# Kernel optimization log

Hardware: AMD Instinct MI355X
Metric: run time of the kernel (lower is better)

The kernel has to match this reference:

```python
import jax, jax.numpy as jnp
import numpy as np
from jax import lax

B, S, C, H, P = 128, 512, 64, 512, 192  # batch, seq_len, enc_in, hidden_size, pred_len


def setup_inputs() -> dict:
    key = jax.random.key(0)
    ks = jax.random.split(key, 9)
    s_enc = 1.0 / np.sqrt(C)
    s_lstm = 1.0 / np.sqrt(H)
    return {
        "x": jax.random.normal(ks[0], (B, S, C), dtype=jnp.float32),
        "enc_W": jax.random.uniform(ks[1], (H, C), jnp.float32, -s_enc, s_enc),
        "enc_b": jax.random.uniform(ks[2], (H,), jnp.float32, -s_enc, s_enc),
        "Wih": jax.random.uniform(ks[3], (4 * H, H), jnp.float32, -s_lstm, s_lstm),
        "Whh": jax.random.uniform(ks[4], (4 * H, H), jnp.float32, -s_lstm, s_lstm),
        "bih": jax.random.uniform(ks[5], (4 * H,), jnp.float32, -s_lstm, s_lstm),
        "bhh": jax.random.uniform(ks[6], (4 * H,), jnp.float32, -s_lstm, s_lstm),
        "dec_W": jax.random.uniform(ks[7], (C, H), jnp.float32, -s_lstm, s_lstm),
        "dec_b": jax.random.uniform(ks[8], (C,), jnp.float32, -s_lstm, s_lstm),
    }


def _gates(pre):
    # PyTorch LSTM gate order: i, f, g, o
    i, f, g, o = jnp.split(pre, 4, axis=-1)
    return jax.nn.sigmoid(i), jax.nn.sigmoid(f), jnp.tanh(g), jax.nn.sigmoid(o)


def reference(x, enc_W, enc_b, Wih, Whh, bih, bhh, dec_W, dec_b):
    b = bih + bhh

    # encoder: [B,S,C] -> [B,S,H]
    xe = x @ enc_W.T + enc_b

    # main LSTM over seq_len with zero init state
    def cell(carry, xt):
        h, c = carry
        i, f, g, o = _gates(xt @ Wih.T + h @ Whh.T + b)
        c2 = f * c + i * g
        h2 = o * jnp.tanh(c2)
        return (h2, c2), h2

    z = jnp.zeros((x.shape[0], Wih.shape[0] // 4), dtype=x.dtype)
    (_, _), outs = lax.scan(cell, (z, z), xe.transpose(1, 0, 2))  # outs: [S,B,H]
    h_last = outs[-1]

    # (torch code calls self.Lstm(h) without passing (h,c)), fed previous h.
    def step(h_prev, _):
        i, f, g, o = _gates(h_prev @ Wih.T + b)  # h-state=0 -> no Whh term
        c2 = i * g  # f*0 + i*g
        h2 = o * jnp.tanh(c2)
        return h2, h2

    _, preds = lax.scan(step, h_last, None, length=P)  # [P,B,H]

    full = jnp.concatenate([outs, preds], axis=0)[1:]  # drop first step: [S+P-1,B,H]
    out = full.transpose(1, 0, 2) @ dec_W.T + dec_b  # [B, S+P-1, C]
    return out
```

## Files before the change

kernel.cpp:

```cpp
#include <hip/hip_runtime.h>
#include <cstdint>
#include <cstddef>


typedef __bf16 bf16x8 __attribute__((ext_vector_type(8)));
typedef float  f32x4  __attribute__((ext_vector_type(4)));

static constexpr unsigned long long SENT = 0x7FC07FC07FC07FC0ULL;

static constexpr size_t SZ_HALL = (size_t)705 * 128 * 512 * 2;
static constexpr size_t SZ_WCAT = (size_t)2048 * 576 * 2;
static constexpr size_t SZ_WIH  = (size_t)2048 * 512 * 2;
static constexpr size_t SZ_DECW = (size_t)64 * 512 * 2;
static constexpr size_t SZ_XT   = (size_t)512 * 128 * 64 * 2;
static constexpr size_t OFF_HALL = 0;
static constexpr size_t OFF_WCAT = OFF_HALL + SZ_HALL;
static constexpr size_t OFF_WIH  = OFF_WCAT + SZ_WCAT;
static constexpr size_t OFF_DECW = OFF_WIH + SZ_WIH;
static constexpr size_t OFF_XT   = OFF_DECW + SZ_DECW;
static constexpr size_t OFF_B2   = OFF_XT + SZ_XT;
static constexpr size_t OFF_BAR_ = OFF_B2 + 2048 * 4;
static constexpr size_t WS_NEEDED = OFF_BAR_ + 2048 * 4;

__device__ __forceinline__ float sigm(float x) { return 1.f / (1.f + __expf(-x)); }
__device__ __forceinline__ float tanh_fast(float x) {
  return 1.f - 2.f / (__expf(2.f * x) + 1.f);
}

__global__ void __launch_bounds__(256)
setup0(const float* __restrict__ x, const float* __restrict__ Wih,
       const float* __restrict__ Whh, const float* __restrict__ bih,
       const float* __restrict__ bhh, const float* __restrict__ decW,
       __bf16* __restrict__ xT, __bf16* __restrict__ Wih_bf,
       __bf16* __restrict__ Wcat, __bf16* __restrict__ decW_bf,
       float* __restrict__ b_ar, __bf16* __restrict__ h_all)
{
  size_t gid = (size_t)blockIdx.x * blockDim.x + threadIdx.x;
  size_t gsz = (size_t)gridDim.x * blockDim.x;
  for (size_t i = gid; i < 4194304u; i += gsz) {
    size_t t = i >> 13, b = (i >> 6) & 127u, c = i & 63u;
    xT[i] = (__bf16)x[(b * 512 + t) * 64 + c];
  }
  for (size_t i = gid; i < 1048576u; i += gsz) Wih_bf[i] = (__bf16)Wih[i];
  for (size_t i = gid; i < 1048576u; i += gsz) {
    size_t r = i >> 9, k = i & 511u;
    Wcat[r * 576 + k] = (__bf16)Whh[i];
  }
  for (size_t i = gid; i < 32768u; i += gsz) decW_bf[i] = (__bf16)decW[i];
  for (size_t i = gid; i < 2048u; i += gsz) b_ar[i] = bih[i] + bhh[i];
  unsigned long long* hp = (unsigned long long*)h_all;
  for (size_t i = gid; i < 16384u; i += gsz) hp[i] = 0ULL;
  for (size_t i = 16384u + gid; i < 11550720u; i += gsz) hp[i] = SENT;
}

__global__ void __launch_bounds__(64)
setup1(const float* __restrict__ Wih, const float* __restrict__ encW,
       const float* __restrict__ encb, const float* __restrict__ bih,
       const float* __restrict__ bhh, __bf16* __restrict__ Wcat,
       float* __restrict__ b2)
{
  int r = blockIdx.x;
  int c = threadIdx.x;
  const float* wr = Wih + (size_t)r * 512;
  float acc = 0.f;
  for (int k = 0; k < 512; ++k) acc += wr[k] * encW[(size_t)k * 64 + c];
  Wcat[(size_t)r * 576 + 512 + c] = (__bf16)acc;
  float p = 0.f;
  for (int kk = 0; kk < 8; ++kk) { int k = kk * 64 + c; p += wr[k] * encb[k]; }
  for (int off = 32; off > 0; off >>= 1) p += __shfl_down(p, off);
  if (c == 0) b2[r] = bih[r] + bhh[r] + p;
}

template<bool MAIN>
__device__ __forceinline__ void lstm_step(
    unsigned t, int tid, int wv, int lane, int n16, int quad, int b0, int f0,
    const bf16x8 (&wf)[18], const f32x4& bv,
    __bf16* __restrict__ h_all, const __bf16* __restrict__ xT,
    float& creg, __bf16 (&A)[16][584], __bf16 (&hb)[16][68])
{
  uint4 xv;
  if (MAIN && tid < 128)
    xv = *(const uint4*)(xT + (size_t)(t - 1) * 8192 +
                         (size_t)(b0 + (tid >> 3)) * 64 + (tid & 7) * 8);

  const unsigned long long* src = (const unsigned long long*)
      (h_all + (size_t)(t - 1) * 65536 + (size_t)(b0 + (tid >> 6)) * 512) +
      (size_t)(tid & 63) * 2;
  unsigned long long v0 = __hip_atomic_load(src,     __ATOMIC_RELAXED, __HIP_MEMORY_SCOPE_AGENT);
  unsigned long long v1 = __hip_atomic_load(src + 1, __ATOMIC_RELAXED, __HIP_MEMORY_SCOPE_AGENT);
  while (v0 == SENT || v1 == SENT) {
    if (v0 == SENT) v0 = __hip_atomic_load(src,     __ATOMIC_RELAXED, __HIP_MEMORY_SCOPE_AGENT);
    if (v1 == SENT) v1 = __hip_atomic_load(src + 1, __ATOMIC_RELAXED, __HIP_MEMORY_SCOPE_AGENT);
  }

  {
    unsigned long long* ad = (unsigned long long*)&A[tid >> 6][(tid & 63) * 8];
    ad[0] = v0; ad[1] = v1;
  }
  if (MAIN && tid < 128)
    *(uint4*)(&A[tid >> 3][512 + (tid & 7) * 8]) = xv;
  __syncthreads();

  f32x4 a0 = bv, a1 = {0.f, 0.f, 0.f, 0.f};
  const __bf16* arow = &A[n16][quad * 8];
  #pragma unroll
  for (int kc = 0; kc < (MAIN ? 18 : 16); ++kc) {
    bf16x8 af = *(const bf16x8*)(arow + kc * 32);
    if (kc & 1) a1 = __builtin_amdgcn_mfma_f32_16x16x32_bf16(wf[kc], af, a1, 0, 0, 0);
    else        a0 = __builtin_amdgcn_mfma_f32_16x16x32_bf16(wf[kc], af, a0, 0, 0, 0);
  }
  a0 += a1;

  float ig = sigm(a0[0]), gg = tanh_fast(a0[2]), og = sigm(a0[3]);
  float c2;
  if (MAIN) { float fg = sigm(a0[1]); c2 = fg * creg + ig * gg; creg = c2; }
  else      { c2 = ig * gg; }
  hb[n16][wv * 4 + quad] = (__bf16)(og * tanh_fast(c2));
  __syncthreads();

  if (tid < 256) {
    const int em = tid >> 4, p = tid & 15;
    unsigned long long pk = *(const unsigned long long*)&hb[em][p * 4];
    unsigned long long* dst = (unsigned long long*)
        (h_all + (size_t)t * 65536 + (size_t)(b0 + em) * 512 + f0) + p;
    __hip_atomic_store(dst, pk, __ATOMIC_RELAXED, __HIP_MEMORY_SCOPE_AGENT);
  }
}

__global__ void __launch_bounds__(1024, 4)
lstm_persist(const __bf16* __restrict__ xT, const __bf16* __restrict__ Wcat,
             const __bf16* __restrict__ Wih_bf, const float* __restrict__ b2,
             const float* __restrict__ b_ar, __bf16* __restrict__ h_all)
{
  const int bid = blockIdx.x;
  const int g = bid & 7, sub = bid >> 3;
  const int b0 = g * 16, f0 = sub * 64;
  const int tid = threadIdx.x;
  const int wv = tid >> 6, lane = tid & 63;
  const int n16 = lane & 15, quad = lane >> 4;

  __shared__ __align__(16) __bf16 A[16][584];
  __shared__ __align__(16) __bf16 hb[16][68];

  bf16x8 wf[18];
  f32x4 bv;
  {
    const int gate = n16 & 3, fl = n16 >> 2;
    const __bf16* wrow = Wcat + (size_t)(gate * 512 + f0 + wv * 4 + fl) * 576 + quad * 8;
    #pragma unroll
    for (int kc = 0; kc < 18; ++kc) wf[kc] = *(const bf16x8*)(wrow + kc * 32);
    const int fb = f0 + wv * 4 + quad;
    bv = f32x4{b2[fb], b2[512 + fb], b2[1024 + fb], b2[1536 + fb]};
  }

  float creg = 0.f;

  for (unsigned t = 1; t <= 512; ++t)
    lstm_step<true>(t, tid, wv, lane, n16, quad, b0, f0, wf, bv,
                    h_all, xT, creg, A, hb);

  {
    const int gate = n16 & 3, fl = n16 >> 2;
    const __bf16* wrow = Wih_bf + (size_t)(gate * 512 + f0 + wv * 4 + fl) * 512 + quad * 8;
    #pragma unroll
    for (int kc = 0; kc < 16; ++kc) wf[kc] = *(const bf16x8*)(wrow + kc * 32);
    const int fb = f0 + wv * 4 + quad;
    bv = f32x4{b_ar[fb], b_ar[512 + fb], b_ar[1024 + fb], b_ar[1536 + fb]};
  }
  for (unsigned t = 513; t <= 704; ++t)
    lstm_step<false>(t, tid, wv, lane, n16, quad, b0, f0, wf, bv,
                     h_all, xT, creg, A, hb);
}

__global__ void __launch_bounds__(256)
final_proj(const __bf16* __restrict__ h_all, const __bf16* __restrict__ decW_bf,
           const float* __restrict__ decb, float* __restrict__ out)
{
  const int bi = blockIdx.x;
  const int tid = threadIdx.x;
  const int wv = tid >> 6, lane = tid & 63;
  const int n16 = lane & 15, quad = lane >> 4;
  const size_t r0 = 256 + (size_t)bi * 128 + (size_t)wv * 32;

  f32x4 acc[2][4];
  #pragma unroll
  for (int mt = 0; mt < 2; ++mt)
    #pragma unroll
    for (int nt = 0; nt < 4; ++nt) acc[mt][nt] = f32x4{0.f, 0.f, 0.f, 0.f};

  const __bf16* arow0 = h_all + (r0 + n16) * 512 + quad * 8;
  const __bf16* arow1 = arow0 + 16 * 512;
  const __bf16* brow  = decW_bf + (size_t)n16 * 512 + quad * 8;

  #pragma unroll
  for (int kc = 0; kc < 16; ++kc) {
    bf16x8 a0 = *(const bf16x8*)(arow0 + kc * 32);
    bf16x8 a1 = *(const bf16x8*)(arow1 + kc * 32);
    #pragma unroll
    for (int nt = 0; nt < 4; ++nt) {
      bf16x8 b = *(const bf16x8*)(brow + (size_t)nt * 8192 + kc * 32);
      acc[0][nt] = __builtin_amdgcn_mfma_f32_16x16x32_bf16(a0, b, acc[0][nt], 0, 0, 0);
      acc[1][nt] = __builtin_amdgcn_mfma_f32_16x16x32_bf16(a1, b, acc[1][nt], 0, 0, 0);
    }
  }
  #pragma unroll
  for (int mt = 0; mt < 2; ++mt)
    #pragma unroll
    for (int nt = 0; nt < 4; ++nt)
      #pragma unroll
      for (int r = 0; r < 4; ++r) {
        size_t R = r0 + mt * 16 + quad * 4 + r;
        int slot = (int)(R >> 7), b = (int)(R & 127);
        int j = slot - 2;
        int c = nt * 16 + n16;
        out[((size_t)b * 703 + j) * 64 + c] = acc[mt][nt][r] + decb[c];
      }
}

extern "C" void kernel_launch(void* const* d_in, const int* in_sizes, int n_in,
                              void* d_out, int out_size, void* d_ws, size_t ws_size,
                              hipStream_t stream)
{
  const float* x    = (const float*)d_in[0];
  const float* encW = (const float*)d_in[1];
  const float* encb = (const float*)d_in[2];
  const float* Wih  = (const float*)d_in[3];
  const float* Whh  = (const float*)d_in[4];
  const float* bih  = (const float*)d_in[5];
  const float* bhh  = (const float*)d_in[6];
  const float* decW = (const float*)d_in[7];
  const float* decb = (const float*)d_in[8];
  float* out = (float*)d_out;

  if (ws_size < WS_NEEDED) return;

  char* ws = (char*)d_ws;
  __bf16* h_all   = (__bf16*)(ws + OFF_HALL);
  __bf16* Wcat    = (__bf16*)(ws + OFF_WCAT);
  __bf16* Wih_bf  = (__bf16*)(ws + OFF_WIH);
  __bf16* decW_bf = (__bf16*)(ws + OFF_DECW);
  __bf16* xT      = (__bf16*)(ws + OFF_XT);
  float*  b2      = (float*)(ws + OFF_B2);
  float*  b_ar    = (float*)(ws + OFF_BAR_);

  hipLaunchKernelGGL(setup0, dim3(2048), dim3(256), 0, stream,
                     x, Wih, Whh, bih, bhh, decW, xT, Wih_bf, Wcat, decW_bf,
                     b_ar, h_all);
  hipLaunchKernelGGL(setup1, dim3(2048), dim3(64), 0, stream,
                     Wih, encW, encb, bih, bhh, Wcat, b2);
  hipLaunchKernelGGL(lstm_persist, dim3(64), dim3(1024), 0, stream,
                     xT, Wcat, Wih_bf, b2, b_ar, h_all);
  hipLaunchKernelGGL(final_proj, dim3(703), dim3(256), 0, stream,
                     h_all, decW_bf, decb, out);
}
```

Measured before the change: 1.840 ms.

## Split LSTM step K-reduction across wave pairs with LDS partial-sum exchange

Each wave now computes half of the K dimension for its own gate tile and half for its partner wave (wv^8), then the pair exchanges partial accumulators through a new shared buffer. Every wave still issues the same number of MFMAs, but the two independent accumulators per wave now cover different output tiles, and each wave reads only half of the A row from LDS. The goal is to shorten the dependent MFMA chain and the LDS read traffic on the serial per-step critical path. The cost is an extra __syncthreads and an LDS round trip of partial sums every timestep.

```diff
diff --git a/kernel.cpp b/kernel.cpp
--- a/kernel.cpp
+++ b/kernel.cpp
@@ -74,10 +74,15 @@
 template<bool MAIN>
 __device__ __forceinline__ void lstm_step(
     unsigned t, int tid, int wv, int lane, int n16, int quad, int b0, int f0,
-    const bf16x8 (&wf)[18], const f32x4& bv,
+    const bf16x8 (&wfo)[9], const bf16x8 (&wfx)[9], const f32x4& bv,
     __bf16* __restrict__ h_all, const __bf16* __restrict__ xT,
-    float& creg, __bf16 (&A)[16][584], __bf16 (&hb)[16][68])
-{
+    float& creg, __bf16 (&A)[16][584], __bf16 (&hb)[16][68],
+    f32x4 (&px)[8][2][64])
+{
+  const int p = wv & 7, r = wv >> 3;
+  const int kb = r * (MAIN ? 9 : 8);
+  constexpr int KH = MAIN ? 9 : 8;
+
   uint4 xv;
   if (MAIN && tid < 128)
     xv = *(const uint4*)(xT + (size_t)(t - 1) * 8192 +
@@ -101,28 +106,31 @@
     *(uint4*)(&A[tid >> 3][512 + (tid & 7) * 8]) = xv;
   __syncthreads();
 
-  f32x4 a0 = bv, a1 = {0.f, 0.f, 0.f, 0.f};
-  const __bf16* arow = &A[n16][quad * 8];
-  #pragma unroll
-  for (int kc = 0; kc < (MAIN ? 18 : 16); ++kc) {
+  f32x4 ao = bv, ax = {0.f, 0.f, 0.f, 0.f};
+  const __bf16* arow = &A[n16][quad * 8 + kb * 32];
+  #pragma unroll
+  for (int kc = 0; kc < KH; ++kc) {
     bf16x8 af = *(const bf16x8*)(arow + kc * 32);
-    if (kc & 1) a1 = __builtin_amdgcn_mfma_f32_16x16x32_bf16(wf[kc], af, a1, 0, 0, 0);
-    else        a0 = __builtin_amdgcn_mfma_f32_16x16x32_bf16(wf[kc], af, a0, 0, 0, 0);
-  }
-  a0 += a1;
-
-  float ig = sigm(a0[0]), gg = tanh_fast(a0[2]), og = sigm(a0[3]);
+    ao = __builtin_amdgcn_mfma_f32_16x16x32_bf16(wfo[kc], af, ao, 0, 0, 0);
+    ax = __builtin_amdgcn_mfma_f32_16x16x32_bf16(wfx[kc], af, ax, 0, 0, 0);
+  }
+
+  px[p][r][lane] = ax;
+  __syncthreads();
+  ao += px[p][r ^ 1][lane];
+
+  float ig = sigm(ao[0]), gg = tanh_fast(ao[2]), og = sigm(ao[3]);
   float c2;
-  if (MAIN) { float fg = sigm(a0[1]); c2 = fg * creg + ig * gg; creg = c2; }
+  if (MAIN) { float fg = sigm(ao[1]); c2 = fg * creg + ig * gg; creg = c2; }
   else      { c2 = ig * gg; }
   hb[n16][wv * 4 + quad] = (__bf16)(og * tanh_fast(c2));
   __syncthreads();
 
   if (tid < 256) {
-    const int em = tid >> 4, p = tid & 15;
-    unsigned long long pk = *(const unsigned long long*)&hb[em][p * 4];
+    const int em = tid >> 4, pp = tid & 15;
+    unsigned long long pk = *(const unsigned long long*)&hb[em][pp * 4];
     unsigned long long* dst = (unsigned long long*)
-        (h_all + (size_t)t * 65536 + (size_t)(b0 + em) * 512 + f0) + p;
+        (h_all + (size_t)t * 65536 + (size_t)(b0 + em) * 512 + f0) + pp;
     __hip_atomic_store(dst, pk, __ATOMIC_RELAXED, __HIP_MEMORY_SCOPE_AGENT);
   }
 }
@@ -141,14 +149,22 @@
 
   __shared__ __align__(16) __bf16 A[16][584];
   __shared__ __align__(16) __bf16 hb[16][68];
-
-  bf16x8 wf[18];
+  __shared__ __align__(16) f32x4 px[8][2][64];
+
+  bf16x8 wfo[9], wfx[9];
   f32x4 bv;
   {
     const int gate = n16 & 3, fl = n16 >> 2;
-    const __bf16* wrow = Wcat + (size_t)(gate * 512 + f0 + wv * 4 + fl) * 576 + quad * 8;
-    #pragma unroll
-    for (int kc = 0; kc < 18; ++kc) wf[kc] = *(const bf16x8*)(wrow + kc * 32);
+    const int kb = (wv >> 3) * 9;
+    const __bf16* wro = Wcat + (size_t)(gate * 512 + f0 + wv * 4 + fl) * 576
+                        + kb * 32 + quad * 8;
+    const __bf16* wrx = Wcat + (size_t)(gate * 512 + f0 + (wv ^ 8) * 4 + fl) * 576
+                        + kb * 32 + quad * 8;
+    #pragma unroll
+    for (int kc = 0; kc < 9; ++kc) {
+      wfo[kc] = *(const bf16x8*)(wro + kc * 32);
+      wfx[kc] = *(const bf16x8*)(wrx + kc * 32);
+    }
     const int fb = f0 + wv * 4 + quad;
     bv = f32x4{b2[fb], b2[512 + fb], b2[1024 + fb], b2[1536 + fb]};
   }
@@ -156,20 +172,27 @@
   float creg = 0.f;
 
   for (unsigned t = 1; t <= 512; ++t)
-    lstm_step<true>(t, tid, wv, lane, n16, quad, b0, f0, wf, bv,
-                    h_all, xT, creg, A, hb);
+    lstm_step<true>(t, tid, wv, lane, n16, quad, b0, f0, wfo, wfx, bv,
+                    h_all, xT, creg, A, hb, px);
 
   {
     const int gate = n16 & 3, fl = n16 >> 2;
-    const __bf16* wrow = Wih_bf + (size_t)(gate * 512 + f0 + wv * 4 + fl) * 512 + quad * 8;
-    #pragma unroll
-    for (int kc = 0; kc < 16; ++kc) wf[kc] = *(const bf16x8*)(wrow + kc * 32);
+    const int kb = (wv >> 3) * 8;
+    const __bf16* wro = Wih_bf + (size_t)(gate * 512 + f0 + wv * 4 + fl) * 512
+                        + kb * 32 + quad * 8;
+    const __bf16* wrx = Wih_bf + (size_t)(gate * 512 + f0 + (wv ^ 8) * 4 + fl) * 512
+                        + kb * 32 + quad * 8;
+    #pragma unroll
+    for (int kc = 0; kc < 8; ++kc) {
+      wfo[kc] = *(const bf16x8*)(wro + kc * 32);
+      wfx[kc] = *(const bf16x8*)(wrx + kc * 32);
+    }
     const int fb = f0 + wv * 4 + quad;
     bv = f32x4{b_ar[fb], b_ar[512 + fb], b_ar[1024 + fb], b_ar[1536 + fb]};
   }
   for (unsigned t = 513; t <= 704; ++t)
-    lstm_step<false>(t, tid, wv, lane, n16, quad, b0, f0, wf, bv,
-                     h_all, xT, creg, A, hb);
+    lstm_step<false>(t, tid, wv, lane, n16, quad, b0, f0, wfo, wfx, bv,
+                     h_all, xT, creg, A, hb, px);
 }
 
 __global__ void __launch_bounds__(256)
```

New measurement: 1.798 ms. 1.02x faster.

## Split LSTM over 128 smaller blocks with feature-quad-major h layout and shuffles

Applied to the files above, without the earlier changes.

The persistent LSTM kernel now runs 128 blocks of 512 threads, each owning 32 hidden features instead of 64, spreading the recurrence over more CUs. The h state buffer is relaid out as [t][feature-quad][batch] 8-byte words, so each wave packs its four gate-lane outputs with cross-lane shuffles and publishes them directly, removing the hb staging buffer and one __syncthreads per step. The A staging tile is double-buffered across steps, and final_proj is rewritten to read the new layout. The trade-off is more blocks polling flags each step and more strided 8-byte loads in the projection.

```diff
diff --git a/kernel.cpp b/kernel.cpp
--- a/kernel.cpp
+++ b/kernel.cpp
@@ -27,6 +27,7 @@
   return 1.f - 2.f / (__expf(2.f * x) + 1.f);
 }
 
+
 __global__ void __launch_bounds__(256)
 setup0(const float* __restrict__ x, const float* __restrict__ Wih,
        const float* __restrict__ Whh, const float* __restrict__ bih,
@@ -76,26 +77,30 @@
     unsigned t, int tid, int wv, int lane, int n16, int quad, int b0, int f0,
     const bf16x8 (&wf)[18], const f32x4& bv,
     __bf16* __restrict__ h_all, const __bf16* __restrict__ xT,
-    float& creg, __bf16 (&A)[16][584], __bf16 (&hb)[16][68])
+    float& creg, __bf16 (*A)[584])
 {
   uint4 xv;
   if (MAIN && tid < 128)
     xv = *(const uint4*)(xT + (size_t)(t - 1) * 8192 +
                          (size_t)(b0 + (tid >> 3)) * 64 + (tid & 7) * 8);
 
-  const unsigned long long* src = (const unsigned long long*)
-      (h_all + (size_t)(t - 1) * 65536 + (size_t)(b0 + (tid >> 6)) * 512) +
-      (size_t)(tid & 63) * 2;
-  unsigned long long v0 = __hip_atomic_load(src,     __ATOMIC_RELAXED, __HIP_MEMORY_SCOPE_AGENT);
-  unsigned long long v1 = __hip_atomic_load(src + 1, __ATOMIC_RELAXED, __HIP_MEMORY_SCOPE_AGENT);
-  while (v0 == SENT || v1 == SENT) {
-    if (v0 == SENT) v0 = __hip_atomic_load(src,     __ATOMIC_RELAXED, __HIP_MEMORY_SCOPE_AGENT);
-    if (v1 == SENT) v1 = __hip_atomic_load(src + 1, __ATOMIC_RELAXED, __HIP_MEMORY_SCOPE_AGENT);
+  const unsigned long long* s0 = (const unsigned long long*)
+      (h_all + (size_t)(t - 1) * 65536) +
+      (size_t)(wv * 16 + (quad << 2)) * 128 + (b0 + n16);
+  unsigned long long v0 = __hip_atomic_load(s0,       __ATOMIC_RELAXED, __HIP_MEMORY_SCOPE_AGENT);
+  unsigned long long v1 = __hip_atomic_load(s0 + 128, __ATOMIC_RELAXED, __HIP_MEMORY_SCOPE_AGENT);
+  unsigned long long v2 = __hip_atomic_load(s0 + 256, __ATOMIC_RELAXED, __HIP_MEMORY_SCOPE_AGENT);
+  unsigned long long v3 = __hip_atomic_load(s0 + 384, __ATOMIC_RELAXED, __HIP_MEMORY_SCOPE_AGENT);
+  while (v0 == SENT || v1 == SENT || v2 == SENT || v3 == SENT) {
+    if (v0 == SENT) v0 = __hip_atomic_load(s0,       __ATOMIC_RELAXED, __HIP_MEMORY_SCOPE_AGENT);
+    if (v1 == SENT) v1 = __hip_atomic_load(s0 + 128, __ATOMIC_RELAXED, __HIP_MEMORY_SCOPE_AGENT);
+    if (v2 == SENT) v2 = __hip_atomic_load(s0 + 256, __ATOMIC_RELAXED, __HIP_MEMORY_SCOPE_AGENT);
+    if (v3 == SENT) v3 = __hip_atomic_load(s0 + 384, __ATOMIC_RELAXED, __HIP_MEMORY_SCOPE_AGENT);
   }
 
   {
-    unsigned long long* ad = (unsigned long long*)&A[tid >> 6][(tid & 63) * 8];
-    ad[0] = v0; ad[1] = v1;
+    unsigned long long* ad = (unsigned long long*)&A[n16][wv * 64 + (quad << 4)];
+    ad[0] = v0; ad[1] = v1; ad[2] = v2; ad[3] = v3;
   }
   if (MAIN && tid < 128)
     *(uint4*)(&A[tid >> 3][512 + (tid & 7) * 8]) = xv;
@@ -115,32 +120,33 @@
   float c2;
   if (MAIN) { float fg = sigm(a0[1]); c2 = fg * creg + ig * gg; creg = c2; }
   else      { c2 = ig * gg; }
-  hb[n16][wv * 4 + quad] = (__bf16)(og * tanh_fast(c2));
-  __syncthreads();
-
-  if (tid < 256) {
-    const int em = tid >> 4, p = tid & 15;
-    unsigned long long pk = *(const unsigned long long*)&hb[em][p * 4];
+  unsigned hbits = __builtin_bit_cast(unsigned short, (__bf16)(og * tanh_fast(c2)));
+
+  unsigned long long pk = 0;
+  #pragma unroll
+  for (int q = 0; q < 4; ++q)
+    pk |= (unsigned long long)(unsigned short)__shfl((int)hbits, q * 16 + n16) << (16 * q);
+  if (lane < 16) {
+    const int fq = (f0 >> 2) + wv;
     unsigned long long* dst = (unsigned long long*)
-        (h_all + (size_t)t * 65536 + (size_t)(b0 + em) * 512 + f0) + p;
+        (h_all + (size_t)t * 65536) + (size_t)fq * 128 + (b0 + lane);
     __hip_atomic_store(dst, pk, __ATOMIC_RELAXED, __HIP_MEMORY_SCOPE_AGENT);
   }
 }
 
-__global__ void __launch_bounds__(1024, 4)
+__global__ void __launch_bounds__(512, 2)
 lstm_persist(const __bf16* __restrict__ xT, const __bf16* __restrict__ Wcat,
              const __bf16* __restrict__ Wih_bf, const float* __restrict__ b2,
              const float* __restrict__ b_ar, __bf16* __restrict__ h_all)
 {
   const int bid = blockIdx.x;
   const int g = bid & 7, sub = bid >> 3;
-  const int b0 = g * 16, f0 = sub * 64;
+  const int b0 = g * 16, f0 = sub * 32;
   const int tid = threadIdx.x;
   const int wv = tid >> 6, lane = tid & 63;
   const int n16 = lane & 15, quad = lane >> 4;
 
-  __shared__ __align__(16) __bf16 A[16][584];
-  __shared__ __align__(16) __bf16 hb[16][68];
+  __shared__ __align__(16) __bf16 Abuf[2][16][584];
 
   bf16x8 wf[18];
   f32x4 bv;
@@ -157,7 +163,7 @@
 
   for (unsigned t = 1; t <= 512; ++t)
     lstm_step<true>(t, tid, wv, lane, n16, quad, b0, f0, wf, bv,
-                    h_all, xT, creg, A, hb);
+                    h_all, xT, creg, Abuf[t & 1]);
 
   {
     const int gate = n16 & 3, fl = n16 >> 2;
@@ -169,7 +175,7 @@
   }
   for (unsigned t = 513; t <= 704; ++t)
     lstm_step<false>(t, tid, wv, lane, n16, quad, b0, f0, wf, bv,
-                     h_all, xT, creg, A, hb);
+                     h_all, xT, creg, Abuf[t & 1]);
 }
 
 __global__ void __launch_bounds__(256)
@@ -182,25 +188,37 @@
   const int n16 = lane & 15, quad = lane >> 4;
   const size_t r0 = 256 + (size_t)bi * 128 + (size_t)wv * 32;
 
+  union U8 { unsigned long long u[2]; bf16x8 v; };
+  const unsigned long long* hq = (const unsigned long long*)h_all;
+
+  size_t base[2];
+  #pragma unroll
+  for (int mt = 0; mt < 2; ++mt) {
+    size_t Rm = r0 + (size_t)mt * 16 + n16;
+    base[mt] = (Rm >> 7) * 16384 + (Rm & 127);
+  }
+
   f32x4 acc[2][4];
   #pragma unroll
   for (int mt = 0; mt < 2; ++mt)
     #pragma unroll
     for (int nt = 0; nt < 4; ++nt) acc[mt][nt] = f32x4{0.f, 0.f, 0.f, 0.f};
 
-  const __bf16* arow0 = h_all + (r0 + n16) * 512 + quad * 8;
-  const __bf16* arow1 = arow0 + 16 * 512;
-  const __bf16* brow  = decW_bf + (size_t)n16 * 512 + quad * 8;
+  const __bf16* brow = decW_bf + (size_t)n16 * 512 + quad * 8;
 
   #pragma unroll
   for (int kc = 0; kc < 16; ++kc) {
-    bf16x8 a0 = *(const bf16x8*)(arow0 + kc * 32);
-    bf16x8 a1 = *(const bf16x8*)(arow1 + kc * 32);
+    const int fq = quad * 2 + kc * 8;
+    U8 a0, a1;
+    a0.u[0] = hq[base[0] + (size_t)fq * 128];
+    a0.u[1] = hq[base[0] + (size_t)(fq + 1) * 128];
+    a1.u[0] = hq[base[1] + (size_t)fq * 128];
+    a1.u[1] = hq[base[1] + (size_t)(fq + 1) * 128];
     #pragma unroll
     for (int nt = 0; nt < 4; ++nt) {
       bf16x8 b = *(const bf16x8*)(brow + (size_t)nt * 8192 + kc * 32);
-      acc[0][nt] = __builtin_amdgcn_mfma_f32_16x16x32_bf16(a0, b, acc[0][nt], 0, 0, 0);
-      acc[1][nt] = __builtin_amdgcn_mfma_f32_16x16x32_bf16(a1, b, acc[1][nt], 0, 0, 0);
+      acc[0][nt] = __builtin_amdgcn_mfma_f32_16x16x32_bf16(a0.v, b, acc[0][nt], 0, 0, 0);
+      acc[1][nt] = __builtin_amdgcn_mfma_f32_16x16x32_bf16(a1.v, b, acc[1][nt], 0, 0, 0);
     }
   }
   #pragma unroll
@@ -248,7 +266,7 @@
                      b_ar, h_all);
   hipLaunchKernelGGL(setup1, dim3(2048), dim3(64), 0, stream,
                      Wih, encW, encb, bih, bhh, Wcat, b2);
-  hipLaunchKernelGGL(lstm_persist, dim3(64), dim3(1024), 0, stream,
+  hipLaunchKernelGGL(lstm_persist, dim3(128), dim3(512), 0, stream,
                      xT, Wcat, Wih_bf, b2, b_ar, h_all);
   hipLaunchKernelGGL(final_proj, dim3(703), dim3(256), 0, stream,
                      h_all, decW_bf, decb, out);
```

Measured after the change: 1.787 ms. 1.03x faster.
